# Optimization experiments

Measured on AMD Instinct MI355X. Metric: run time of the kernel, lower is better.

Reference implementation:

```python
import jax, jax.numpy as jnp
import numpy as np

D_MODEL = 1024
N_HEADS = 16
D_K = D_MODEL // N_HEADS
D_FF = 4096
EPS = 1e-5


def layer_norm(x, gamma, beta):
    mu = jnp.mean(x, axis=-1, keepdims=True)
    var = jnp.var(x, axis=-1, keepdims=True)
    return (x - mu) * jax.lax.rsqrt(var + EPS) * gamma + beta


def setup_inputs() -> dict:
    key = jax.random.key(0)
    ks = jax.random.split(key, 16)
    B, S = 4, 1024
    s = 0.02
    inp = {
        "x": jax.random.normal(ks[0], (B, S, D_MODEL), dtype=jnp.float32),
        "mask": jnp.ones((B, 1, 1, S), dtype=jnp.int32),
        "Wq": jax.random.normal(ks[1], (D_MODEL, D_MODEL), jnp.float32) * s,
        "bq": jnp.zeros((D_MODEL,), jnp.float32),
        "Wk": jax.random.normal(ks[2], (D_MODEL, D_MODEL), jnp.float32) * s,
        "bk": jnp.zeros((D_MODEL,), jnp.float32),
        "Wv": jax.random.normal(ks[3], (D_MODEL, D_MODEL), jnp.float32) * s,
        "bv": jnp.zeros((D_MODEL,), jnp.float32),
        "Wo": jax.random.normal(ks[4], (D_MODEL, D_MODEL), jnp.float32) * s,
        "bo": jnp.zeros((D_MODEL,), jnp.float32),
        "W1": jax.random.normal(ks[5], (D_MODEL, D_FF), jnp.float32) * s,
        "b1": jnp.zeros((D_FF,), jnp.float32),
        "W2": jax.random.normal(ks[6], (D_FF, D_MODEL), jnp.float32) * s,
        "b2": jnp.zeros((D_MODEL,), jnp.float32),
        "ln1_g": jnp.ones((D_MODEL,), jnp.float32),
        "ln1_b": jnp.zeros((D_MODEL,), jnp.float32),
        "ln2_g": jnp.ones((D_MODEL,), jnp.float32),
        "ln2_b": jnp.zeros((D_MODEL,), jnp.float32),
    }
    return inp


def reference(x, mask, Wq, bq, Wk, bk, Wv, bv, Wo, bo, W1, b1, W2, b2,
              ln1_g, ln1_b, ln2_g, ln2_b):
    B, S, _ = x.shape
    # QKV projections -> [B, H, S, d_k]
    def split_heads(t):
        return t.reshape(B, S, N_HEADS, D_K).transpose(0, 2, 1, 3)
    Q = split_heads(x @ Wq + bq)
    K = split_heads(x @ Wk + bk)
    V = split_heads(x @ Wv + bv)
    # scores [B, H, S, S]
    scores = jnp.einsum('bhqd,bhkd->bhqk', Q, K) / jnp.sqrt(jnp.float32(D_K))
    scores = jnp.where(mask == 0, jnp.float32(-1e9), scores)
    attn = jax.nn.softmax(scores, axis=-1)
    ctx = jnp.einsum('bhqk,bhkd->bhqd', attn, V)
    ctx = ctx.transpose(0, 2, 1, 3).reshape(B, S, D_MODEL)
    attn_out = ctx @ Wo + bo
    # residual + LN (dropout is identity in eval)
    h = layer_norm(x + attn_out, ln1_g, ln1_b)
    ff = jax.nn.relu(h @ W1 + b1) @ W2 + b2
    return layer_norm(h + ff, ln2_g, ln2_b)
```

## Files before the change

### kernel.cpp

```cpp
#include <hip/hip_runtime.h>
#include <hip/hip_bf16.h>

typedef __attribute__((ext_vector_type(8))) short bf16x8;
typedef __attribute__((ext_vector_type(4))) float f32x4;
typedef __attribute__((ext_vector_type(16))) float f32x16;
typedef unsigned int u32;
typedef unsigned short ush;

#define SEQ 1024
#define MTOT 4096
#define QSCALE_LOG2 0.18033688f

#if __has_builtin(__builtin_amdgcn_exp2f)
#define EXP2(x) __builtin_amdgcn_exp2f(x)
#else
#define EXP2(x) exp2f(x)
#endif

__device__ __forceinline__ ush f2bf(float f){
  u32 u = __float_as_uint(f);
  u32 r = (u + 0x7fffu + ((u >> 16) & 1u)) >> 16;
  return (ush)r;
}

__device__ __forceinline__ f32x4 mfma16(bf16x8 a, bf16x8 b, f32x4 c){
  return __builtin_amdgcn_mfma_f32_16x16x32_bf16(a, b, c, 0, 0, 0);
}
__device__ __forceinline__ f32x16 mfma32(bf16x8 a, bf16x8 b, f32x16 c){
  return __builtin_amdgcn_mfma_f32_32x32x16_bf16(a, b, c, 0, 0, 0);
}

__device__ __forceinline__ u32 cvtpk(float lo, float hi){
  u32 r; asm("v_cvt_pk_bf16_f32 %0, %1, %2" : "=v"(r) : "v"(lo), "v"(hi)); return r;
}

__device__ __forceinline__ void gload_lds16(const ush* g, ush* l){
  __builtin_amdgcn_global_load_lds(
      (const __attribute__((address_space(1))) u32*)g,
      (__attribute__((address_space(3))) u32*)l, 16, 0, 0);
}

__global__ __launch_bounds__(256) void cvt_kernel(const float* __restrict__ src,
                                                  ush* __restrict__ dst, int n){
  int i = (blockIdx.x * 256 + threadIdx.x) * 4;
  if (i < n){
    float4 v = *(const float4*)&src[i];
    ushort4 o = { f2bf(v.x), f2bf(v.y), f2bf(v.z), f2bf(v.w) };
    *(ushort4*)&dst[i] = o;
  }
}

__global__ __launch_bounds__(256) void tconv_kernel(const float* __restrict__ src,
                                                    ush* __restrict__ dst, int R, int C){
  __shared__ float t[32][33];
  int tx = threadIdx.x & 31, ty = threadIdx.x >> 5;
  int r0 = blockIdx.y * 32, c0 = blockIdx.x * 32;
  #pragma unroll
  for (int i = 0; i < 32; i += 8)
    t[ty + i][tx] = src[(size_t)(r0 + ty + i) * C + (c0 + tx)];
  __syncthreads();
  #pragma unroll
  for (int i = 0; i < 32; i += 8)
    dst[(size_t)(c0 + ty + i) * R + (r0 + tx)] = f2bf(t[tx][ty + i]);
}

__global__ __launch_bounds__(256) void biaspack_kernel(const float* __restrict__ bq,
    const float* __restrict__ bk, const float* __restrict__ bv, float* __restrict__ dst){
  int i = blockIdx.x * 256 + threadIdx.x;
  if (i < 3072){
    float v = (i < 1024) ? bq[i] : (i < 2048) ? bk[i - 1024] : bv[i - 2048];
    dst[i] = v;
  }
}

__global__ __launch_bounds__(256) void vtrans_kernel(const ush* __restrict__ qkv,
                                                     ush* __restrict__ VT){
  __shared__ ush t[32][34];
  int tx = threadIdx.x & 31, ty = threadIdx.x >> 5;
  int bh = blockIdx.z, b = bh >> 4, h = bh & 15;
  int k0 = blockIdx.x * 32, d0 = blockIdx.y * 32;
  #pragma unroll
  for (int i = 0; i < 32; i += 8)
    t[ty + i][tx] = qkv[(size_t)(b * SEQ + k0 + ty + i) * 3072 + 2048 + h * 64 + d0 + tx];
  __syncthreads();
  #pragma unroll
  for (int i = 0; i < 32; i += 8)
    VT[(size_t)(bh * 64 + d0 + ty + i) * SEQ + k0 + tx] = t[tx][ty + i];
}

__device__ __forceinline__ void stage_piece(ush* piece, const ush* g0, int K,
                                            int tid, int w){
  #pragma unroll
  for (int I = 0; I < 2; I++){
    int c = I * 512 + tid;
    int r = c >> 2;
    int gl = (c & 3) ^ ((r >> 1) & 3);
    gload_lds16(g0 + (size_t)r * K + gl * 8, piece + I * 4096 + w * 512);
  }
}

__device__ __forceinline__ bf16x8 frag(const ush* piece, int row, int g){
  int phys = g ^ ((row >> 1) & 3);
  return *(const bf16x8*)(piece + row * 32 + phys * 8);
}

#define PH_BAR_TOP() do{ __builtin_amdgcn_sched_barrier(0); \
  __builtin_amdgcn_s_barrier(); \
  asm volatile("s_waitcnt lgkmcnt(0)" ::: "memory"); \
  __builtin_amdgcn_sched_barrier(0); \
  __builtin_amdgcn_s_setprio(1); }while(0)
#define PH_BAR_BOT() do{ __builtin_amdgcn_s_setprio(0); \
  __builtin_amdgcn_sched_barrier(0); \
  __builtin_amdgcn_s_barrier(); }while(0)

template<int RELU, int OUTF32, int SCALEQ>
__global__ __launch_bounds__(512, 2) void gemm8_kernel(
    const ush* __restrict__ A, const ush* __restrict__ Bt,
    const float* __restrict__ bias,
    ush* __restrict__ Cb, float* __restrict__ Cf,
    int M, int N, int K, int ldc, int ksl)
{
  __shared__ ush lds[2][2][2][8192];
  const int tid = threadIdx.x;
  const int lane = tid & 63, w = tid >> 6;
  const int g = lane >> 4, qr = lane & 15;
  const int wr = w >> 2, wc = w & 3;
  const int gx = gridDim.x;
  const int nwg = gx * gridDim.y;
  const int id = blockIdx.y * gx + blockIdx.x;
  const int swz = (id & 7) * (nwg >> 3) + (id >> 3);
  const int bn = (swz % gx) * 256;
  const int bm = (swz / gx) * 256;
  const int kbase = blockIdx.z * ksl;
  const int NT = ksl >> 6;
  const ush* Ab = A  + (size_t)bm * K + kbase;
  const ush* Bb = Bt + (size_t)bn * K + kbase;

  stage_piece(lds[0][0][0], Ab,      K, tid, w);
  stage_piece(lds[0][1][0], Bb,      K, tid, w);
  stage_piece(lds[0][0][1], Ab + 32, K, tid, w);
  stage_piece(lds[0][1][1], Bb + 32, K, tid, w);
  if (NT > 1){
    stage_piece(lds[1][0][0], Ab + 64, K, tid, w);
    stage_piece(lds[1][1][0], Bb + 64, K, tid, w);
  }
  asm volatile("s_waitcnt vmcnt(4)" ::: "memory");
  __builtin_amdgcn_sched_barrier(0);
  __builtin_amdgcn_s_barrier();

  f32x4 acc[8][4] = {};
  const int ar = wr * 128 + qr;
  const int br = wc * 64 + qr;

  for (int T = 0; T < NT; ++T){
    const int cb = T & 1, nb = cb ^ 1;
    const ush* An = Ab + (size_t)(T + 1) * 64;
    const ush* Bn = Bb + (size_t)(T + 1) * 64;
    const ush* Af = Ab + (size_t)(T + 2) * 64;
    const ush* Bf = Bb + (size_t)(T + 2) * 64;
    bf16x8 af[4], bfr[4];

    #pragma unroll
    for (int j = 0; j < 4; j++) bfr[j] = frag(lds[cb][1][0], br + j * 16, g);
    #pragma unroll
    for (int i = 0; i < 4; i++) af[i] = frag(lds[cb][0][0], ar + i * 16, g);
    if (T + 1 < NT) stage_piece(lds[nb][0][1], An + 32, K, tid, w);
    PH_BAR_TOP();
    #pragma unroll
    for (int i = 0; i < 4; i++)
      #pragma unroll
      for (int j = 0; j < 4; j++)
        acc[i][j] = mfma16(af[i], bfr[j], acc[i][j]);
    PH_BAR_BOT();

    #pragma unroll
    for (int i = 0; i < 4; i++) af[i] = frag(lds[cb][0][0], ar + 64 + i * 16, g);
    if (T + 1 < NT) stage_piece(lds[nb][1][1], Bn + 32, K, tid, w);
    PH_BAR_TOP();
    #pragma unroll
    for (int i = 0; i < 4; i++)
      #pragma unroll
      for (int j = 0; j < 4; j++)
        acc[4 + i][j] = mfma16(af[i], bfr[j], acc[4 + i][j]);
    PH_BAR_BOT();

    #pragma unroll
    for (int j = 0; j < 4; j++) bfr[j] = frag(lds[cb][1][1], br + j * 16, g);
    #pragma unroll
    for (int i = 0; i < 4; i++) af[i] = frag(lds[cb][0][1], ar + i * 16, g);
    if (T + 2 < NT) stage_piece(lds[cb][0][0], Af, K, tid, w);
    PH_BAR_TOP();
    #pragma unroll
    for (int i = 0; i < 4; i++)
      #pragma unroll
      for (int j = 0; j < 4; j++)
        acc[i][j] = mfma16(af[i], bfr[j], acc[i][j]);
    PH_BAR_BOT();

    #pragma unroll
    for (int i = 0; i < 4; i++) af[i] = frag(lds[cb][0][1], ar + 64 + i * 16, g);
    if (T + 2 < NT) stage_piece(lds[cb][1][0], Bf, K, tid, w);
    PH_BAR_TOP();
    #pragma unroll
    for (int i = 0; i < 4; i++)
      #pragma unroll
      for (int j = 0; j < 4; j++)
        acc[4 + i][j] = mfma16(af[i], bfr[j], acc[4 + i][j]);
    __builtin_amdgcn_s_setprio(0);
    __builtin_amdgcn_sched_barrier(0);
    asm volatile("s_waitcnt vmcnt(4)" ::: "memory");
    __builtin_amdgcn_sched_barrier(0);
    __builtin_amdgcn_s_barrier();
  }

  float* Cfz = Cf;
  if (OUTF32) Cfz = Cf + (size_t)blockIdx.z * M * ldc;
  #pragma unroll
  for (int j = 0; j < 4; j++){
    const int col = bn + wc * 64 + j * 16 + qr;
    const float bv = OUTF32 ? 0.f : bias[col];
    const float scl = (SCALEQ && col < 1024) ? QSCALE_LOG2 : 1.f;
    #pragma unroll
    for (int i = 0; i < 8; i++){
      const int row0 = bm + wr * 128 + i * 16 + g * 4;
      #pragma unroll
      for (int rr = 0; rr < 4; rr++){
        float v = acc[i][j][rr] + bv;
        if (RELU) v = fmaxf(v, 0.f);
        if (SCALEQ) v *= scl;
        const size_t idx = (size_t)(row0 + rr) * ldc + col;
        if (OUTF32) Cfz[idx] = v; else Cb[idx] = f2bf(v);
      }
    }
  }
}

__global__ __launch_bounds__(256) void attn2_kernel(
    const ush* __restrict__ qkv, const ush* __restrict__ VT,
    const int* __restrict__ mask, ush* __restrict__ ctx)
{
  const int tid = threadIdx.x;
  const int lane = tid & 63, w = tid >> 6;
  const int c = lane & 31, hi = lane >> 5;
  const int bh = blockIdx.y, b = bh >> 4, hh = bh & 15;
  const int q0 = blockIdx.x * 128 + w * 32;

  __shared__ int mflag;
  if (tid == 0) mflag = 1;
  __syncthreads();
  {
    int4 mv = *(const int4*)&mask[b * SEQ + tid * 4];
    if (!(mv.x && mv.y && mv.z && mv.w)) mflag = 0;
  }
  __syncthreads();
  const bool maskall = (mflag != 0);

  const ush* Qrow = qkv + (size_t)(b * SEQ + q0 + c) * 3072 + hh * 64;
  bf16x8 qf[4];
  #pragma unroll
  for (int kd = 0; kd < 4; kd++)
    qf[kd] = *(const bf16x8*)(Qrow + kd * 16 + hi * 8);

  const ush* Kb  = qkv + (size_t)(b * SEQ) * 3072 + 1024 + hh * 64;
  const ush* VTb = VT + (size_t)(bh * 64) * SEQ;

  f32x16 o0 = {}, o1 = {};
  float m_run = -1e30f, l_run = 0.f;

  bf16x8 kf[8];
  #pragma unroll
  for (int kb = 0; kb < 2; kb++)
    #pragma unroll
    for (int kd = 0; kd < 4; kd++)
      kf[kb * 4 + kd] = *(const bf16x8*)(Kb + (size_t)(kb * 32 + c) * 3072 + kd * 16 + hi * 8);

  for (int t = 0; t < SEQ / 64; ++t){
    const int k0 = t * 64;
    bf16x8 vf[8];
    #pragma unroll
    for (int db = 0; db < 2; db++)
      #pragma unroll
      for (int ks = 0; ks < 4; ks++)
        vf[db * 4 + ks] = *(const bf16x8*)(VTb + (size_t)(db * 32 + c) * SEQ + k0 + ks * 16 + hi * 8);

    f32x16 s0 = {}, s1 = {};
    #pragma unroll
    for (int kd = 0; kd < 4; kd++){
      s0 = mfma32(kf[kd],     qf[kd], s0);
      s1 = mfma32(kf[4 + kd], qf[kd], s1);
    }

    float p[32];
    #pragma unroll
    for (int r = 0; r < 16; r++){ p[r] = s0[r]; p[16 + r] = s1[r]; }

    if (!maskall){
      #pragma unroll
      for (int r32 = 0; r32 < 32; r32++){
        int r = r32 & 15;
        int key = (r32 >> 4) * 32 + (r & 3) + 8 * (r >> 2) + 4 * hi;
        if (mask[b * SEQ + k0 + key] == 0) p[r32] = -1e9f;
      }
    }

    if (t + 1 < SEQ / 64){
      #pragma unroll
      for (int kb = 0; kb < 2; kb++)
        #pragma unroll
        for (int kd = 0; kd < 4; kd++)
          kf[kb * 4 + kd] = *(const bf16x8*)(Kb + (size_t)(k0 + 64 + kb * 32 + c) * 3072 + kd * 16 + hi * 8);
    }

    float pmax = p[0];
    #pragma unroll
    for (int r = 1; r < 32; r++) pmax = fmaxf(pmax, p[r]);
    pmax = fmaxf(pmax, __shfl_xor(pmax, 32));
    if (__any(pmax > m_run + 8.f)){
      float m_new = fmaxf(m_run, pmax);
      float corr = EXP2(m_run - m_new);
      l_run *= corr;
      m_run = m_new;
      #pragma unroll
      for (int r = 0; r < 16; r++){
        float cr = __shfl(corr, (r & 3) + 8 * (r >> 2) + 4 * hi);
        o0[r] *= cr; o1[r] *= cr;
      }
    }
    float ls = 0.f;
    #pragma unroll
    for (int r = 0; r < 32; r++){ p[r] = EXP2(p[r] - m_run); ls += p[r]; }
    ls += __shfl_xor(ls, 32);
    l_run += ls;

    union { u32 wdw[4]; bf16x8 v; } af[4];
    #pragma unroll
    for (int ks = 0; ks < 4; ks++){
      int b0 = (ks >> 1) * 16 + 8 * (ks & 1);
      u32 c00 = cvtpk(p[b0],     p[b0 + 1]);
      u32 c01 = cvtpk(p[b0 + 2], p[b0 + 3]);
      u32 c10 = cvtpk(p[b0 + 4], p[b0 + 5]);
      u32 c11 = cvtpk(p[b0 + 6], p[b0 + 7]);
      asm volatile("v_permlane32_swap_b32 %0, %1" : "+v"(c10), "+v"(c00));
      asm volatile("v_permlane32_swap_b32 %0, %1" : "+v"(c11), "+v"(c01));
      af[ks].wdw[0] = c00; af[ks].wdw[1] = c01; af[ks].wdw[2] = c10; af[ks].wdw[3] = c11;
    }

    #pragma unroll
    for (int ks = 0; ks < 4; ks++){
      o0 = mfma32(af[ks].v, vf[ks],     o0);
      o1 = mfma32(af[ks].v, vf[4 + ks], o1);
    }
  }

  float linv = 1.f / l_run;
  #pragma unroll
  for (int r = 0; r < 16; r++){
    int crow = (r & 3) + 8 * (r >> 2) + 4 * hi;
    float li = __shfl(linv, crow);
    size_t base = (size_t)(b * SEQ + q0 + crow) * 1024 + hh * 64;
    ctx[base + c]      = f2bf(o0[r] * li);
    ctx[base + 32 + c] = f2bf(o1[r] * li);
  }
}

template<bool WB>
__global__ __launch_bounds__(256) void ln4_kernel(
    const float* __restrict__ X, const float* __restrict__ P,
    const float* __restrict__ bias,
    const float* __restrict__ gam, const float* __restrict__ bet,
    float* __restrict__ Of, ush* __restrict__ Ob)
{
  const int row = blockIdx.x, tid = threadIdx.x;
  const size_t base = (size_t)row * 1024 + tid * 4;
  float4 xv = *(const float4*)&X[base];
  float4 bv4 = *(const float4*)&bias[tid * 4];
  float s0 = xv.x + bv4.x, s1 = xv.y + bv4.y, s2 = xv.z + bv4.z, s3 = xv.w + bv4.w;
  #pragma unroll
  for (int z = 0; z < 4; z++){
    float4 p = *(const float4*)&P[(size_t)z * 4194304 + base];
    s0 += p.x; s1 += p.y; s2 += p.z; s3 += p.w;
  }
  float sum = s0 + s1 + s2 + s3;
  float sq  = s0 * s0 + s1 * s1 + s2 * s2 + s3 * s3;
  #pragma unroll
  for (int o = 1; o < 64; o <<= 1){ sum += __shfl_xor(sum, o); sq += __shfl_xor(sq, o); }
  __shared__ float red[8];
  int lane = tid & 63, w = tid >> 6;
  if (lane == 0){ red[w] = sum; red[4 + w] = sq; }
  __syncthreads();
  sum = red[0] + red[1] + red[2] + red[3];
  sq  = red[4] + red[5] + red[6] + red[7];
  float mean = sum * (1.f / 1024.f);
  float var  = sq * (1.f / 1024.f) - mean * mean;
  float rs = rsqrtf(var + 1e-5f);
  float4 gv = *(const float4*)&gam[tid * 4];
  float4 bt = *(const float4*)&bet[tid * 4];
  float o0 = (s0 - mean) * rs * gv.x + bt.x;
  float o1 = (s1 - mean) * rs * gv.y + bt.y;
  float o2 = (s2 - mean) * rs * gv.z + bt.z;
  float o3 = (s3 - mean) * rs * gv.w + bt.w;
  float4 ov = { o0, o1, o2, o3 };
  *(float4*)&Of[base] = ov;
  if (WB){
    ushort4 ob = { f2bf(o0), f2bf(o1), f2bf(o2), f2bf(o3) };
    *(ushort4*)&Ob[base] = ob;
  }
}

extern "C" void kernel_launch(void* const* d_in, const int* in_sizes, int n_in,
                              void* d_out, int out_size, void* d_ws, size_t ws_size,
                              hipStream_t stream)
{
  const float* x    = (const float*)d_in[0];
  const int*   mask = (const int*)  d_in[1];
  const float* Wq = (const float*)d_in[2];
  const float* bq = (const float*)d_in[3];
  const float* Wk = (const float*)d_in[4];
  const float* bk = (const float*)d_in[5];
  const float* Wv = (const float*)d_in[6];
  const float* bv = (const float*)d_in[7];
  const float* Wo = (const float*)d_in[8];
  const float* bo = (const float*)d_in[9];
  const float* W1 = (const float*)d_in[10];
  const float* b1 = (const float*)d_in[11];
  const float* W2 = (const float*)d_in[12];
  const float* b2 = (const float*)d_in[13];
  const float* g1 = (const float*)d_in[14];
  const float* be1= (const float*)d_in[15];
  const float* g2 = (const float*)d_in[16];
  const float* be2= (const float*)d_in[17];
  float* out = (float*)d_out;

  char* ws = (char*)d_ws;
  size_t off = 0;
  auto alloc = [&](size_t bytes)->void*{ void* p = ws + off; off += (bytes + 255) & ~(size_t)255; return p; };
  ush* xb     = (ush*)alloc((size_t)MTOT * 1024 * 2);
  ush* wqkvT  = (ush*)alloc((size_t)3072 * 1024 * 2);
  ush* woT    = (ush*)alloc((size_t)1024 * 1024 * 2);
  ush* w1T    = (ush*)alloc((size_t)4096 * 1024 * 2);
  ush* w2T    = (ush*)alloc((size_t)1024 * 4096 * 2);
  float* bqkv = (float*)alloc(3072 * 4);
  ush* qkv    = (ush*)alloc((size_t)MTOT * 3072 * 2);
  ush* ctx    = (ush*)alloc((size_t)MTOT * 1024 * 2);
  float* part = (float*)alloc((size_t)4 * MTOT * 1024 * 4);
  float* h    = (float*)alloc((size_t)MTOT * 1024 * 4);
  ush* hb     = (ush*)alloc((size_t)MTOT * 1024 * 2);
  ush* VT     = (ush*)alloc((size_t)64 * 64 * SEQ * 2);
  ush* ff1    = qkv;

  cvt_kernel<<<dim3(4096), dim3(256), 0, stream>>>(x, xb, MTOT * 1024);
  tconv_kernel<<<dim3(32, 32), dim3(256), 0, stream>>>(Wq, wqkvT,               1024, 1024);
  tconv_kernel<<<dim3(32, 32), dim3(256), 0, stream>>>(Wk, wqkvT + 1024 * 1024, 1024, 1024);
  tconv_kernel<<<dim3(32, 32), dim3(256), 0, stream>>>(Wv, wqkvT + 2048 * 1024, 1024, 1024);
  tconv_kernel<<<dim3(32, 32), dim3(256), 0, stream>>>(Wo, woT,                 1024, 1024);
  tconv_kernel<<<dim3(128, 32), dim3(256), 0, stream>>>(W1, w1T, 1024, 4096);
  tconv_kernel<<<dim3(32, 128), dim3(256), 0, stream>>>(W2, w2T, 4096, 1024);
  biaspack_kernel<<<dim3(12), dim3(256), 0, stream>>>(bq, bk, bv, bqkv);

  gemm8_kernel<0, 0, 1><<<dim3(12, 16, 1), dim3(512), 0, stream>>>(
      xb, wqkvT, bqkv, qkv, nullptr, MTOT, 3072, 1024, 3072, 1024);

  vtrans_kernel<<<dim3(32, 2, 64), dim3(256), 0, stream>>>(qkv, VT);

  attn2_kernel<<<dim3(8, 64), dim3(256), 0, stream>>>(qkv, VT, mask, ctx);

  gemm8_kernel<0, 1, 0><<<dim3(4, 16, 4), dim3(512), 0, stream>>>(
      ctx, woT, nullptr, nullptr, part, MTOT, 1024, 1024, 1024, 256);

  ln4_kernel<true><<<dim3(4096), dim3(256), 0, stream>>>(x, part, bo, g1, be1, h, hb);

  gemm8_kernel<1, 0, 0><<<dim3(16, 16, 1), dim3(512), 0, stream>>>(
      hb, w1T, b1, ff1, nullptr, MTOT, 4096, 1024, 4096, 1024);

  gemm8_kernel<0, 1, 0><<<dim3(4, 16, 4), dim3(512), 0, stream>>>(
      ff1, w2T, nullptr, nullptr, part, MTOT, 1024, 4096, 1024, 1024);

  ln4_kernel<false><<<dim3(4096), dim3(256), 0, stream>>>(h, part, b2, g2, be2, out, nullptr);
}
```

Measured before the change: 390.4 us.

## Split attention over two key halves with a combine kernel

The attention kernel now processes each query tile over half of the keys (split-K flash-decoding style), doubling the grid from 512 to 1024 blocks. It writes unnormalised fp32 partial outputs plus running max and sum, and a new combine kernel merges the two halves and converts the result to bf16. It also raises MFMA wave priority around the matrix ops and replaces the serial max and sum reductions with tree reductions. The aim is better CU occupancy on the attention step, at the cost of extra fp32 traffic (about 32MB written and read) and one more launch.

```diff
diff --git a/kernel.cpp b/kernel.cpp
--- a/kernel.cpp
+++ b/kernel.cpp
@@ -235,14 +235,17 @@
   }
 }
 
-__global__ __launch_bounds__(256) void attn2_kernel(
+__global__ __launch_bounds__(256, 4) void attn2_kernel(
     const ush* __restrict__ qkv, const ush* __restrict__ VT,
-    const int* __restrict__ mask, ush* __restrict__ ctx)
+    const int* __restrict__ mask, float* __restrict__ Opart,
+    float* __restrict__ ml)
 {
   const int tid = threadIdx.x;
   const int lane = tid & 63, w = tid >> 6;
   const int c = lane & 31, hi = lane >> 5;
-  const int bh = blockIdx.y, b = bh >> 4, hh = bh & 15;
+  const int bh = blockIdx.z, b = bh >> 4, hh = bh & 15;
+  const int split = blockIdx.y;
+  const int kbeg = split * 512;
   const int q0 = blockIdx.x * 128 + w * 32;
 
   __shared__ int mflag;
@@ -272,10 +275,10 @@
   for (int kb = 0; kb < 2; kb++)
     #pragma unroll
     for (int kd = 0; kd < 4; kd++)
-      kf[kb * 4 + kd] = *(const bf16x8*)(Kb + (size_t)(kb * 32 + c) * 3072 + kd * 16 + hi * 8);
-
-  for (int t = 0; t < SEQ / 64; ++t){
-    const int k0 = t * 64;
+      kf[kb * 4 + kd] = *(const bf16x8*)(Kb + (size_t)(kbeg + kb * 32 + c) * 3072 + kd * 16 + hi * 8);
+
+  for (int t = 0; t < 8; ++t){
+    const int k0 = kbeg + t * 64;
     bf16x8 vf[8];
     #pragma unroll
     for (int db = 0; db < 2; db++)
@@ -284,11 +287,13 @@
         vf[db * 4 + ks] = *(const bf16x8*)(VTb + (size_t)(db * 32 + c) * SEQ + k0 + ks * 16 + hi * 8);
 
     f32x16 s0 = {}, s1 = {};
+    __builtin_amdgcn_s_setprio(1);
     #pragma unroll
     for (int kd = 0; kd < 4; kd++){
       s0 = mfma32(kf[kd],     qf[kd], s0);
       s1 = mfma32(kf[4 + kd], qf[kd], s1);
     }
+    __builtin_amdgcn_s_setprio(0);
 
     float p[32];
     #pragma unroll
@@ -303,7 +308,7 @@
       }
     }
 
-    if (t + 1 < SEQ / 64){
+    if (t + 1 < 8){
       #pragma unroll
       for (int kb = 0; kb < 2; kb++)
         #pragma unroll
@@ -311,10 +316,15 @@
           kf[kb * 4 + kd] = *(const bf16x8*)(Kb + (size_t)(k0 + 64 + kb * 32 + c) * 3072 + kd * 16 + hi * 8);
     }
 
-    float pmax = p[0];
-    #pragma unroll
-    for (int r = 1; r < 32; r++) pmax = fmaxf(pmax, p[r]);
-    pmax = fmaxf(pmax, __shfl_xor(pmax, 32));
+    float tm[16];
+    #pragma unroll
+    for (int r = 0; r < 16; r++) tm[r] = fmaxf(p[r], p[r + 16]);
+    #pragma unroll
+    for (int s = 8; s >= 1; s >>= 1)
+      #pragma unroll
+      for (int r = 0; r < s; r++) tm[r] = fmaxf(tm[r], tm[r + s]);
+    float pmax = fmaxf(tm[0], __shfl_xor(tm[0], 32));
+
     if (__any(pmax > m_run + 8.f)){
       float m_new = fmaxf(m_run, pmax);
       float corr = EXP2(m_run - m_new);
@@ -326,11 +336,19 @@
         o0[r] *= cr; o1[r] *= cr;
       }
     }
-    float ls = 0.f;
-    #pragma unroll
-    for (int r = 0; r < 32; r++){ p[r] = EXP2(p[r] - m_run); ls += p[r]; }
-    ls += __shfl_xor(ls, 32);
-    l_run += ls;
+
+    float ts[16];
+    #pragma unroll
+    for (int r = 0; r < 16; r++){
+      p[r]      = EXP2(p[r] - m_run);
+      p[r + 16] = EXP2(p[r + 16] - m_run);
+      ts[r] = p[r] + p[r + 16];
+    }
+    #pragma unroll
+    for (int s = 8; s >= 1; s >>= 1)
+      #pragma unroll
+      for (int r = 0; r < s; r++) ts[r] += ts[r + s];
+    l_run += ts[0] + __shfl_xor(ts[0], 32);
 
     union { u32 wdw[4]; bf16x8 v; } af[4];
     #pragma unroll
@@ -345,22 +363,52 @@
       af[ks].wdw[0] = c00; af[ks].wdw[1] = c01; af[ks].wdw[2] = c10; af[ks].wdw[3] = c11;
     }
 
+    __builtin_amdgcn_s_setprio(1);
     #pragma unroll
     for (int ks = 0; ks < 4; ks++){
       o0 = mfma32(af[ks].v, vf[ks],     o0);
       o1 = mfma32(af[ks].v, vf[4 + ks], o1);
     }
-  }
-
-  float linv = 1.f / l_run;
+    __builtin_amdgcn_s_setprio(0);
+  }
+
+  if (lane < 32){
+    float2* mlp = (float2*)ml;
+    mlp[((size_t)split * 64 + bh) * SEQ + q0 + c] = make_float2(m_run, l_run);
+  }
   #pragma unroll
   for (int r = 0; r < 16; r++){
     int crow = (r & 3) + 8 * (r >> 2) + 4 * hi;
-    float li = __shfl(linv, crow);
-    size_t base = (size_t)(b * SEQ + q0 + crow) * 1024 + hh * 64;
-    ctx[base + c]      = f2bf(o0[r] * li);
-    ctx[base + 32 + c] = f2bf(o1[r] * li);
-  }
+    size_t base = (size_t)split * MTOT * 1024 + (size_t)(b * SEQ + q0 + crow) * 1024 + hh * 64;
+    Opart[base + c]      = o0[r];
+    Opart[base + 32 + c] = o1[r];
+  }
+}
+
+__global__ __launch_bounds__(256) void attn_combine_kernel(
+    const float* __restrict__ Opart, const float* __restrict__ ml,
+    ush* __restrict__ ctx)
+{
+  const int row = blockIdx.x;
+  const int b = row >> 10, q = row & 1023;
+  const int col = threadIdx.x * 4;
+  const int hh = col >> 6;
+  const int bh = b * 16 + hh;
+  const float2* mlp = (const float2*)ml;
+  float2 a0 = mlp[(size_t)bh * SEQ + q];
+  float2 a1 = mlp[((size_t)64 + bh) * SEQ + q];
+  float m = fmaxf(a0.x, a1.x);
+  float w0 = EXP2(a0.x - m), w1 = EXP2(a1.x - m);
+  float li = 1.f / fmaxf(a0.y * w0 + a1.y * w1, 1e-30f);
+  size_t base = (size_t)row * 1024 + col;
+  float4 u = *(const float4*)&Opart[base];
+  float4 v = *(const float4*)&Opart[(size_t)MTOT * 1024 + base];
+  ushort4 o;
+  o.x = f2bf((u.x * w0 + v.x * w1) * li);
+  o.y = f2bf((u.y * w0 + v.y * w1) * li);
+  o.z = f2bf((u.z * w0 + v.z * w1) * li);
+  o.w = f2bf((u.w * w0 + v.w * w1) * li);
+  *(ushort4*)&ctx[base] = o;
 }
 
 template<bool WB>
@@ -447,6 +495,8 @@
   ush* hb     = (ush*)alloc((size_t)MTOT * 1024 * 2);
   ush* VT     = (ush*)alloc((size_t)64 * 64 * SEQ * 2);
   ush* ff1    = qkv;
+  float* Opart = part;
+  float* mlbuf = part + (size_t)2 * MTOT * 1024;
 
   cvt_kernel<<<dim3(4096), dim3(256), 0, stream>>>(x, xb, MTOT * 1024);
   tconv_kernel<<<dim3(32, 32), dim3(256), 0, stream>>>(Wq, wqkvT,               1024, 1024);
@@ -462,7 +512,8 @@
 
   vtrans_kernel<<<dim3(32, 2, 64), dim3(256), 0, stream>>>(qkv, VT);
 
-  attn2_kernel<<<dim3(8, 64), dim3(256), 0, stream>>>(qkv, VT, mask, ctx);
+  attn2_kernel<<<dim3(8, 2, 64), dim3(256), 0, stream>>>(qkv, VT, mask, Opart, mlbuf);
+  attn_combine_kernel<<<dim3(4096), dim3(256), 0, stream>>>(Opart, mlbuf, ctx);
 
   gemm8_kernel<0, 1, 0><<<dim3(4, 16, 4), dim3(512), 0, stream>>>(
       ctx, woT, nullptr, nullptr, part, MTOT, 1024, 1024, 1024, 256);
```

Result: slower. 485.2 us (+24.3%).
